# Kernel optimization log

Hardware: AMD Instinct MI355X
Metric: run time of the kernel (lower is better)

## Reference

```python
import jax, jax.numpy as jnp
import numpy as np

N = 100000      # nodes (size_src == size_dst)
E = 1_600_000   # edges, avg degree 16
IN = 128
HID = 128
OUT = 64
DROP_P = 0.5


def setup_inputs() -> dict:
    key = jax.random.key(0)
    ks = jax.random.split(key, 10)
    x = jax.random.normal(ks[0], (N, IN), dtype=jnp.float32)
    edge = jax.random.randint(ks[1], (2, E), 0, N, dtype=jnp.int32)
    # CuGraphSAGEConv: Linear(2*in_channels -> out_channels) over concat([agg, x]), with bias
    def lin_init(k, fan_in, fan_out):
        return jax.random.normal(k, (fan_in, fan_out), dtype=jnp.float32) / np.sqrt(fan_in)
    w0 = lin_init(ks[2], 2 * IN, HID); b0 = jnp.zeros((HID,), jnp.float32)
    w1 = lin_init(ks[3], 2 * HID, HID); b1 = jnp.zeros((HID,), jnp.float32)
    w2 = lin_init(ks[4], 2 * HID, HID); b2 = jnp.zeros((HID,), jnp.float32)
    lin_w = lin_init(ks[5], HID, OUT); lin_b = jnp.zeros((OUT,), jnp.float32)
    return {"x": x, "edge": edge, "w0": w0, "b0": b0, "w1": w1, "b1": b1,
            "w2": w2, "b2": b2, "lin_w": lin_w, "lin_b": lin_b,
            "size_src": N, "size_dst": N}


def _mean_agg(h, src, dst, n):
    # mean over incoming neighbors: agg[i] = mean_{(s->i) in E} h[s]
    msg = jnp.take(h, src, axis=0)                      # [E, d]
    s = jax.ops.segment_sum(msg, dst, num_segments=n)   # [n, d]
    deg = jax.ops.segment_sum(jnp.ones((src.shape[0],), h.dtype), dst, num_segments=n)
    return s / jnp.maximum(deg, 1.0)[:, None]


def _sage_layer(h, src, dst, n_dst, w, b, drop_key):
    agg = _mean_agg(h, src, dst, h.shape[0])            # [n, d]
    z = jnp.concatenate([agg, h], axis=-1) @ w + b      # [n, out]
    z = z[:n_dst]
    z = jax.nn.relu(z)
    keep = jax.random.bernoulli(drop_key, 1.0 - DROP_P, z.shape)
    return jnp.where(keep, z / (1.0 - DROP_P), 0.0)


def reference(x, edge, w0, b0, w1, b1, w2, b2, lin_w, lin_b, size_src, size_dst):
    src, dst = edge[0], edge[1]
    dkey = jax.random.key(42)
    h = x
    for i, (w, b) in enumerate([(w0, b0), (w1, b1), (w2, b2)]):
        h = _sage_layer(h, src, dst, size_dst, w, b, jax.random.fold_in(dkey, i))
    return h @ lin_w + lin_b
```

## Files before the change

### kernel.cpp

```cpp
#include <hip/hip_runtime.h>
#include <stdint.h>

#define NN 100000
#define NE 1600000
#define NFLAT 12800000u
#define XRANGE 12500
#define XCHUNKS 782
#define GBLK 782
#define MAXDEG 64

typedef _Float16 f16;
typedef __attribute__((ext_vector_type(2))) _Float16 f16x2;
typedef __attribute__((ext_vector_type(4))) _Float16 f16x4;
typedef __attribute__((ext_vector_type(8))) _Float16 f16x8;
typedef __attribute__((ext_vector_type(4))) float f32x4;

__device__ __forceinline__ uint32_t rotl32(uint32_t x, int r) {
  return __builtin_amdgcn_alignbit(x, x, (32 - r) & 31);
}

__device__ __forceinline__ void tf2x32(uint32_t k0, uint32_t k1,
                                       uint32_t x0, uint32_t x1,
                                       uint32_t &o0, uint32_t &o1) {
  uint32_t ks2 = k0 ^ k1 ^ 0x1BD11BDAu;
#define TF_R(r) { x0 += x1; x1 = rotl32(x1, r); x1 ^= x0; }
  x0 += k0; x1 += k1;
  TF_R(13) TF_R(15) TF_R(26) TF_R(6)
  x0 += k1;  x1 += ks2 + 1u;
  TF_R(17) TF_R(29) TF_R(16) TF_R(24)
  x0 += ks2; x1 += k0 + 2u;
  TF_R(13) TF_R(15) TF_R(26) TF_R(6)
  x0 += k0;  x1 += k1 + 3u;
  TF_R(17) TF_R(29) TF_R(16) TF_R(24)
  x0 += k1;  x1 += ks2 + 4u;
  TF_R(13) TF_R(15) TF_R(26) TF_R(6)
  x0 += ks2; x1 += k0 + 5u;
#undef TF_R
  o0 = x0; o1 = x1;
}

static void tf2x32_host(uint32_t k0, uint32_t k1, uint32_t x0, uint32_t x1,
                        uint32_t *o0, uint32_t *o1) {
  uint32_t ks2 = k0 ^ k1 ^ 0x1BD11BDAu;
#define TF_R(r) { x0 += x1; x1 = (x1 << (r)) | (x1 >> (32 - (r))); x1 ^= x0; }
  x0 += k0; x1 += k1;
  TF_R(13) TF_R(15) TF_R(26) TF_R(6)
  x0 += k1;  x1 += ks2 + 1u;
  TF_R(17) TF_R(29) TF_R(16) TF_R(24)
  x0 += ks2; x1 += k0 + 2u;
  TF_R(13) TF_R(15) TF_R(26) TF_R(6)
  x0 += k0;  x1 += k1 + 3u;
  TF_R(17) TF_R(29) TF_R(16) TF_R(24)
  x0 += k1;  x1 += ks2 + 4u;
  TF_R(13) TF_R(15) TF_R(26) TF_R(6)
  x0 += ks2; x1 += k0 + 5u;
#undef TF_R
  *o0 = x0; *o1 = x1;
}

__global__ __launch_bounds__(256) void fill_xcd(const int *__restrict__ src,
                                                const int *__restrict__ dst,
                                                int *__restrict__ cursor,
                                                int *__restrict__ col2) {
  int x = blockIdx.x & 7;
  int chunk = blockIdx.x >> 3;
  int lo = x * XRANGE, hi = lo + XRANGE;
  int base = chunk * 2048 + threadIdx.x;
#pragma unroll
  for (int t = 0; t < 8; ++t) {
    int e = base + t * 256;
    if (e < NE) {
      int d = dst[e];
      if (d >= lo && d < hi) {
        int p = atomicAdd(&cursor[d], 1);
        if (p < MAXDEG) col2[d * MAXDEG + p] = src[e];
      }
    }
  }
}

__global__ __launch_bounds__(256) void cvt_x_kernel(const float *__restrict__ x,
                                                    f16 *__restrict__ xh) {
  uint32_t i = (blockIdx.x * 256 + threadIdx.x) * 4;
  float4 v = *(const float4 *)(x + i);
  f16x4 o;
  o[0] = (f16)v.x; o[1] = (f16)v.y; o[2] = (f16)v.z; o[3] = (f16)v.w;
  *(f16x4 *)(xh + i) = o;
}

__global__ __launch_bounds__(256) void cvt_w_kernel(
    const float *__restrict__ w0, const float *__restrict__ w1,
    const float *__restrict__ w2, const float *__restrict__ lw,
    f16 *__restrict__ Wk0, f16 *__restrict__ Wk1, f16 *__restrict__ Wk2,
    f16 *__restrict__ WkL) {
  int t = blockIdx.x * 256 + threadIdx.x;
  if (t < 3 * 32768) {
    int wi = t >> 15, r = t & 32767;
    int k = r >> 7, c = r & 127;
    const float *w = (wi == 0) ? w0 : ((wi == 1) ? w1 : w2);
    f16 *o = (wi == 0) ? Wk0 : ((wi == 1) ? Wk1 : Wk2);
    o[c * 256 + k] = (f16)w[r];
  } else {
    int r = t - 3 * 32768;
    int k = r >> 6, c = r & 63;
    WkL[c * 128 + k] = (f16)lw[r];
  }
}

__global__ __launch_bounds__(256) void agg_kernel(const f16 *__restrict__ h,
                                                  const int *__restrict__ deg,
                                                  const int *__restrict__ col2,
                                                  f16 *__restrict__ agg,
                                                  uint32_t *__restrict__ mrow,
                                                  uint32_t mk0, uint32_t mk1) {
  int wid = threadIdx.x >> 6;
  int lane = threadIdx.x & 63;
  int n = (blockIdx.x & 7) * XRANGE + (blockIdx.x >> 3) * 4 + wid;

  {
    uint32_t j0 = (uint32_t)n * 128u + (uint32_t)lane;
    uint32_t o0, o1, p0, p1;
    tf2x32(mk0, mk1, 0u, j0, o0, o1);
    tf2x32(mk0, mk1, 0u, j0 + 64u, p0, p1);
    unsigned long long blo = __ballot((int)(o0 ^ o1) >= 0);
    unsigned long long bhi = __ballot((int)(p0 ^ p1) >= 0);
    if (lane == 0) {
      uint4 mv;
      mv.x = (uint32_t)blo; mv.y = (uint32_t)(blo >> 32);
      mv.z = (uint32_t)bhi; mv.w = (uint32_t)(bhi >> 32);
      *(uint4 *)(mrow + (size_t)n * 4) = mv;
    }
  }

  const int beg = n * MAXDEG;
  int d = min(deg[n], MAXDEG);
  const int q4 = lane >> 4;
  const int r = lane & 15;
  float s0 = 0.f, s1 = 0.f, s2 = 0.f, s3 = 0.f;
  float s4 = 0.f, s5 = 0.f, s6 = 0.f, s7 = 0.f;
  int i = 0;
  for (; i + 8 <= d; i += 8) {
    int c0 = col2[beg + i + q4];
    int c1 = col2[beg + i + 4 + q4];
    f16x8 v0 = ((const f16x8 *)(h + (size_t)c0 * 128))[r];
    f16x8 v1 = ((const f16x8 *)(h + (size_t)c1 * 128))[r];
    s0 += (float)v0[0] + (float)v1[0];
    s1 += (float)v0[1] + (float)v1[1];
    s2 += (float)v0[2] + (float)v1[2];
    s3 += (float)v0[3] + (float)v1[3];
    s4 += (float)v0[4] + (float)v1[4];
    s5 += (float)v0[5] + (float)v1[5];
    s6 += (float)v0[6] + (float)v1[6];
    s7 += (float)v0[7] + (float)v1[7];
  }
  for (; i + 4 <= d; i += 4) {
    int c = col2[beg + i + q4];
    f16x8 v = ((const f16x8 *)(h + (size_t)c * 128))[r];
    s0 += (float)v[0]; s1 += (float)v[1];
    s2 += (float)v[2]; s3 += (float)v[3];
    s4 += (float)v[4]; s5 += (float)v[5];
    s6 += (float)v[6]; s7 += (float)v[7];
  }
  if (i < d && q4 < d - i) {
    int c = col2[beg + i + q4];
    f16x8 v = ((const f16x8 *)(h + (size_t)c * 128))[r];
    s0 += (float)v[0]; s1 += (float)v[1];
    s2 += (float)v[2]; s3 += (float)v[3];
    s4 += (float)v[4]; s5 += (float)v[5];
    s6 += (float)v[6]; s7 += (float)v[7];
  }
  s0 += __shfl_xor(s0, 16); s0 += __shfl_xor(s0, 32);
  s1 += __shfl_xor(s1, 16); s1 += __shfl_xor(s1, 32);
  s2 += __shfl_xor(s2, 16); s2 += __shfl_xor(s2, 32);
  s3 += __shfl_xor(s3, 16); s3 += __shfl_xor(s3, 32);
  s4 += __shfl_xor(s4, 16); s4 += __shfl_xor(s4, 32);
  s5 += __shfl_xor(s5, 16); s5 += __shfl_xor(s5, 32);
  s6 += __shfl_xor(s6, 16); s6 += __shfl_xor(s6, 32);
  s7 += __shfl_xor(s7, 16); s7 += __shfl_xor(s7, 32);
  if (q4 == 0) {
    float inv = 1.0f / (float)max(d, 1);
    f16x8 o;
    o[0] = (f16)(s0 * inv); o[1] = (f16)(s1 * inv);
    o[2] = (f16)(s2 * inv); o[3] = (f16)(s3 * inv);
    o[4] = (f16)(s4 * inv); o[5] = (f16)(s5 * inv);
    o[6] = (f16)(s6 * inv); o[7] = (f16)(s7 * inv);
    ((f16x8 *)(agg + (size_t)n * 128))[r] = o;
  }
}

__global__ __launch_bounds__(256) void sage_gemm_f16(
    const f16 *__restrict__ agg, const f16 *__restrict__ hin,
    const f16 *__restrict__ Wk, const float *__restrict__ bias,
    const uint32_t *__restrict__ mask, f16 *__restrict__ hout) {
  const int tid = threadIdx.x;
  const int lane = tid & 63;
  const int wv = tid >> 6;
  const int blk_row0 = blockIdx.x * 128;
  const int kg = (lane >> 4) * 8;
  const int col_lo = lane & 15;

  f16x8 Bf[2][8];
#pragma unroll
  for (int t = 0; t < 2; ++t) {
    const int colb = wv * 32 + t * 16 + col_lo;
#pragma unroll
    for (int ks = 0; ks < 8; ++ks)
      Bf[t][ks] = *(const f16x8 *)(Wk + (size_t)colb * 256 + ks * 32 + kg);
  }
  const float bv0 = bias[wv * 32 + col_lo];
  const float bv1 = bias[wv * 32 + 16 + col_lo];

#pragma unroll 2
  for (int s = 0; s < 8; ++s) {
    const int row0 = blk_row0 + s * 16;
    const int ar = row0 + col_lo;
    const bool rowok = ar < NN;
    f16x8 Af[8];
#pragma unroll
    for (int ks = 0; ks < 8; ++ks) {
      const f16 *asrc = (ks < 4)
                            ? (agg + (size_t)ar * 128 + ks * 32 + kg)
                            : (hin + (size_t)ar * 128 + (ks - 4) * 32 + kg);
      Af[ks] = rowok ? *(const f16x8 *)asrc : (f16x8){};
    }
    f32x4 acc0 = {0.f, 0.f, 0.f, 0.f}, acc1 = {0.f, 0.f, 0.f, 0.f};
#pragma unroll
    for (int ks = 0; ks < 8; ++ks) {
      acc0 = __builtin_amdgcn_mfma_f32_16x16x32_f16(Af[ks], Bf[0][ks], acc0, 0, 0, 0);
      acc1 = __builtin_amdgcn_mfma_f32_16x16x32_f16(Af[ks], Bf[1][ks], acc1, 0, 0, 0);
    }
    const int rbase = row0 + (lane >> 4) * 4;
    const int c0 = wv * 32 + col_lo;
    const int c1 = c0 + 16;
#pragma unroll
    for (int r = 0; r < 4; ++r) {
      const int row = rbase + r;
      if (row < NN) {
        uint32_t mw = mask[(size_t)row * 4 + wv];
        float z0 = acc0[r] + bv0;
        float z1 = acc1[r] + bv1;
        z0 = (z0 > 0.f && ((mw >> col_lo) & 1u)) ? z0 * 2.f : 0.f;
        z1 = (z1 > 0.f && ((mw >> (16 + col_lo)) & 1u)) ? z1 * 2.f : 0.f;
        hout[(size_t)row * 128 + c0] = (f16)z0;
        hout[(size_t)row * 128 + c1] = (f16)z1;
      }
    }
  }
}

__global__ __launch_bounds__(256) void final_gemm_f16(
    const f16 *__restrict__ hin, const f16 *__restrict__ WkL,
    const float *__restrict__ bias, float *__restrict__ outp) {
  const int tid = threadIdx.x;
  const int lane = tid & 63;
  const int wv = tid >> 6;
  const int blk_row0 = blockIdx.x * 128;
  const int kg = (lane >> 4) * 8;
  const int col_lo = lane & 15;
  const int c = wv * 16 + col_lo;
  f16x8 Bf[4];
#pragma unroll
  for (int ks = 0; ks < 4; ++ks)
    Bf[ks] = *(const f16x8 *)(WkL + (size_t)c * 128 + ks * 32 + kg);
  const float bv = bias[c];
#pragma unroll 2
  for (int s = 0; s < 8; ++s) {
    const int row0 = blk_row0 + s * 16;
    const int ar = row0 + col_lo;
    const bool rowok = ar < NN;
    f32x4 acc = {0.f, 0.f, 0.f, 0.f};
#pragma unroll
    for (int ks = 0; ks < 4; ++ks) {
      f16x8 a = rowok
                    ? *(const f16x8 *)(hin + (size_t)ar * 128 + ks * 32 + kg)
                    : (f16x8){};
      acc = __builtin_amdgcn_mfma_f32_16x16x32_f16(a, Bf[ks], acc, 0, 0, 0);
    }
    const int rbase = row0 + (lane >> 4) * 4;
#pragma unroll
    for (int r = 0; r < 4; ++r) {
      const int row = rbase + r;
      if (row < NN) outp[(size_t)row * 64 + c] = acc[r] + bv;
    }
  }
}

extern "C" void kernel_launch(void *const *d_in, const int *in_sizes, int n_in,
                              void *d_out, int out_size, void *d_ws,
                              size_t ws_size, hipStream_t stream) {
  (void)in_sizes; (void)n_in; (void)out_size; (void)ws_size;
  const float *x = (const float *)d_in[0];
  const int *edge = (const int *)d_in[1];
  const int *src = edge;
  const int *dst = edge + NE;
  const float *w0 = (const float *)d_in[2];
  const float *b0 = (const float *)d_in[3];
  const float *w1 = (const float *)d_in[4];
  const float *b1 = (const float *)d_in[5];
  const float *w2 = (const float *)d_in[6];
  const float *b2 = (const float *)d_in[7];
  const float *lw = (const float *)d_in[8];
  const float *lb = (const float *)d_in[9];
  float *out = (float *)d_out;

  char *ws = (char *)d_ws;
  f16 *xh  = (f16 *)ws; ws += (size_t)NN * 128 * 2;
  f16 *h1  = (f16 *)ws; ws += (size_t)NN * 128 * 2;
  f16 *h2  = (f16 *)ws; ws += (size_t)NN * 128 * 2;
  f16 *agg = (f16 *)ws; ws += (size_t)NN * 128 * 2;
  f16 *Wk0 = (f16 *)ws; ws += 256 * 128 * 2;
  f16 *Wk1 = (f16 *)ws; ws += 256 * 128 * 2;
  f16 *Wk2 = (f16 *)ws; ws += 256 * 128 * 2;
  f16 *WkL = (f16 *)ws; ws += 128 * 64 * 2;
  int *cursor = (int *)ws; ws += (size_t)NN * 4;
  int *col2 = (int *)ws;   ws += (size_t)NN * MAXDEG * 4;
  uint32_t *m0 = (uint32_t *)ws; ws += (size_t)(NFLAT / 32) * 4;
  uint32_t *m1 = (uint32_t *)ws; ws += (size_t)(NFLAT / 32) * 4;
  uint32_t *m2 = (uint32_t *)ws; ws += (size_t)(NFLAT / 32) * 4;

  uint32_t fk[3][2];
  for (int i = 0; i < 3; ++i)
    tf2x32_host(0u, 42u, 0u, (uint32_t)i, &fk[i][0], &fk[i][1]);

  hipMemsetAsync(cursor, 0, (size_t)NN * 4, stream);
  fill_xcd<<<8 * XCHUNKS, 256, 0, stream>>>(src, dst, cursor, col2);
  cvt_x_kernel<<<NFLAT / 1024, 256, 0, stream>>>(x, xh);
  cvt_w_kernel<<<416, 256, 0, stream>>>(w0, w1, w2, lw, Wk0, Wk1, Wk2, WkL);

  agg_kernel<<<NN / 4, 256, 0, stream>>>(xh, cursor, col2, agg, m0,
                                         fk[0][0], fk[0][1]);
  sage_gemm_f16<<<GBLK, 256, 0, stream>>>(agg, xh, Wk0, b0, m0, h1);
  agg_kernel<<<NN / 4, 256, 0, stream>>>(h1, cursor, col2, agg, m1,
                                         fk[1][0], fk[1][1]);
  sage_gemm_f16<<<GBLK, 256, 0, stream>>>(agg, h1, Wk1, b1, m1, h2);
  agg_kernel<<<NN / 4, 256, 0, stream>>>(h2, cursor, col2, agg, m2,
                                         fk[2][0], fk[2][1]);
  sage_gemm_f16<<<GBLK, 256, 0, stream>>>(agg, h2, Wk2, b2, m2, xh);
  final_gemm_f16<<<GBLK, 256, 0, stream>>>(xh, WkL, lb, out);
}
```

Baseline: 445.3 us.

## Merge prep kernels, fuse final linear into last SAGE GEMM via LDS

Combines the CSR fill, x conversion and weight conversion kernels into one launch partitioned by block index. The final output GEMM is fused into the last SAGE layer's GEMM: the layer-3 activations are staged in shared memory and multiplied by the output weights in the same block, so they are never written to or reread from global memory. The aggregation kernel also gains a 16-neighbor unrolled loop to keep more gathers in flight. Costs are extra LDS use and a block barrier in the fused kernel, plus possible register pressure from the wider unroll.

```diff
diff --git a/kernel.cpp b/kernel.cpp
--- a/kernel.cpp
+++ b/kernel.cpp
@@ -8,6 +8,10 @@
 #define XCHUNKS 782
 #define GBLK 782
 #define MAXDEG 64
+#define FILLB (8 * XCHUNKS)
+#define CVTXB 12500
+#define CVTWB 416
+#define LDSW 136
 
 typedef _Float16 f16;
 typedef __attribute__((ext_vector_type(2))) _Float16 f16x2;
@@ -58,52 +62,51 @@
   *o0 = x0; *o1 = x1;
 }
 
-__global__ __launch_bounds__(256) void fill_xcd(const int *__restrict__ src,
-                                                const int *__restrict__ dst,
-                                                int *__restrict__ cursor,
-                                                int *__restrict__ col2) {
-  int x = blockIdx.x & 7;
-  int chunk = blockIdx.x >> 3;
-  int lo = x * XRANGE, hi = lo + XRANGE;
-  int base = chunk * 2048 + threadIdx.x;
-#pragma unroll
-  for (int t = 0; t < 8; ++t) {
-    int e = base + t * 256;
-    if (e < NE) {
-      int d = dst[e];
-      if (d >= lo && d < hi) {
-        int p = atomicAdd(&cursor[d], 1);
-        if (p < MAXDEG) col2[d * MAXDEG + p] = src[e];
-      }
-    }
-  }
-}
-
-__global__ __launch_bounds__(256) void cvt_x_kernel(const float *__restrict__ x,
-                                                    f16 *__restrict__ xh) {
-  uint32_t i = (blockIdx.x * 256 + threadIdx.x) * 4;
-  float4 v = *(const float4 *)(x + i);
-  f16x4 o;
-  o[0] = (f16)v.x; o[1] = (f16)v.y; o[2] = (f16)v.z; o[3] = (f16)v.w;
-  *(f16x4 *)(xh + i) = o;
-}
-
-__global__ __launch_bounds__(256) void cvt_w_kernel(
+__global__ __launch_bounds__(256) void prep_kernel(
+    const int *__restrict__ src, const int *__restrict__ dst,
+    int *__restrict__ cursor, int *__restrict__ col2,
+    const float *__restrict__ x, f16 *__restrict__ xh,
     const float *__restrict__ w0, const float *__restrict__ w1,
     const float *__restrict__ w2, const float *__restrict__ lw,
     f16 *__restrict__ Wk0, f16 *__restrict__ Wk1, f16 *__restrict__ Wk2,
     f16 *__restrict__ WkL) {
-  int t = blockIdx.x * 256 + threadIdx.x;
-  if (t < 3 * 32768) {
-    int wi = t >> 15, r = t & 32767;
-    int k = r >> 7, c = r & 127;
-    const float *w = (wi == 0) ? w0 : ((wi == 1) ? w1 : w2);
-    f16 *o = (wi == 0) ? Wk0 : ((wi == 1) ? Wk1 : Wk2);
-    o[c * 256 + k] = (f16)w[r];
+  const int bid = blockIdx.x;
+  const int tid = threadIdx.x;
+  if (bid < FILLB) {
+    int xr = bid & 7;
+    int chunk = bid >> 3;
+    int lo = xr * XRANGE, hi = lo + XRANGE;
+    int base = chunk * 2048 + tid;
+#pragma unroll
+    for (int t = 0; t < 8; ++t) {
+      int e = base + t * 256;
+      if (e < NE) {
+        int d = dst[e];
+        if (d >= lo && d < hi) {
+          int p = atomicAdd(&cursor[d], 1);
+          if (p < MAXDEG) col2[d * MAXDEG + p] = src[e];
+        }
+      }
+    }
+  } else if (bid < FILLB + CVTXB) {
+    uint32_t i = (uint32_t)(bid - FILLB) * 1024u + (uint32_t)tid * 4u;
+    float4 v = *(const float4 *)(x + i);
+    f16x4 o;
+    o[0] = (f16)v.x; o[1] = (f16)v.y; o[2] = (f16)v.z; o[3] = (f16)v.w;
+    *(f16x4 *)(xh + i) = o;
   } else {
-    int r = t - 3 * 32768;
-    int k = r >> 6, c = r & 63;
-    WkL[c * 128 + k] = (f16)lw[r];
+    int t = (bid - FILLB - CVTXB) * 256 + tid;
+    if (t < 3 * 32768) {
+      int wi = t >> 15, r = t & 32767;
+      int k = r >> 7, c = r & 127;
+      const float *w = (wi == 0) ? w0 : ((wi == 1) ? w1 : w2);
+      f16 *o = (wi == 0) ? Wk0 : ((wi == 1) ? Wk1 : Wk2);
+      o[c * 256 + k] = (f16)w[r];
+    } else {
+      int r = t - 3 * 32768;
+      int k = r >> 6, c = r & 63;
+      WkL[c * 128 + k] = (f16)lw[r];
+    }
   }
 }
 
@@ -139,6 +142,24 @@
   float s0 = 0.f, s1 = 0.f, s2 = 0.f, s3 = 0.f;
   float s4 = 0.f, s5 = 0.f, s6 = 0.f, s7 = 0.f;
   int i = 0;
+  for (; i + 16 <= d; i += 16) {
+    int c0 = col2[beg + i + q4];
+    int c1 = col2[beg + i + 4 + q4];
+    int c2 = col2[beg + i + 8 + q4];
+    int c3 = col2[beg + i + 12 + q4];
+    f16x8 v0 = ((const f16x8 *)(h + (size_t)c0 * 128))[r];
+    f16x8 v1 = ((const f16x8 *)(h + (size_t)c1 * 128))[r];
+    f16x8 v2 = ((const f16x8 *)(h + (size_t)c2 * 128))[r];
+    f16x8 v3 = ((const f16x8 *)(h + (size_t)c3 * 128))[r];
+    s0 += (float)v0[0] + (float)v1[0] + (float)v2[0] + (float)v3[0];
+    s1 += (float)v0[1] + (float)v1[1] + (float)v2[1] + (float)v3[1];
+    s2 += (float)v0[2] + (float)v1[2] + (float)v2[2] + (float)v3[2];
+    s3 += (float)v0[3] + (float)v1[3] + (float)v2[3] + (float)v3[3];
+    s4 += (float)v0[4] + (float)v1[4] + (float)v2[4] + (float)v3[4];
+    s5 += (float)v0[5] + (float)v1[5] + (float)v2[5] + (float)v3[5];
+    s6 += (float)v0[6] + (float)v1[6] + (float)v2[6] + (float)v3[6];
+    s7 += (float)v0[7] + (float)v1[7] + (float)v2[7] + (float)v3[7];
+  }
   for (; i + 8 <= d; i += 8) {
     int c0 = col2[beg + i + q4];
     int c1 = col2[beg + i + 4 + q4];
@@ -188,10 +209,15 @@
   }
 }
 
+template <int FINAL>
 __global__ __launch_bounds__(256) void sage_gemm_f16(
     const f16 *__restrict__ agg, const f16 *__restrict__ hin,
     const f16 *__restrict__ Wk, const float *__restrict__ bias,
-    const uint32_t *__restrict__ mask, f16 *__restrict__ hout) {
+    const uint32_t *__restrict__ mask, f16 *__restrict__ hout,
+    const f16 *__restrict__ WkL, const float *__restrict__ lb,
+    float *__restrict__ outp) {
+  extern __shared__ char smem[];
+  f16 (*hl)[LDSW] = (f16(*)[LDSW])smem;
   const int tid = threadIdx.x;
   const int lane = tid & 63;
   const int wv = tid >> 6;
@@ -231,7 +257,6 @@
     }
     const int rbase = row0 + (lane >> 4) * 4;
     const int c0 = wv * 32 + col_lo;
-    const int c1 = c0 + 16;
 #pragma unroll
     for (int r = 0; r < 4; ++r) {
       const int row = rbase + r;
@@ -241,46 +266,41 @@
         float z1 = acc1[r] + bv1;
         z0 = (z0 > 0.f && ((mw >> col_lo) & 1u)) ? z0 * 2.f : 0.f;
         z1 = (z1 > 0.f && ((mw >> (16 + col_lo)) & 1u)) ? z1 * 2.f : 0.f;
-        hout[(size_t)row * 128 + c0] = (f16)z0;
-        hout[(size_t)row * 128 + c1] = (f16)z1;
+        if constexpr (FINAL) {
+          const int lr = row - blk_row0;
+          hl[lr][c0] = (f16)z0;
+          hl[lr][c0 + 16] = (f16)z1;
+        } else {
+          hout[(size_t)row * 128 + c0] = (f16)z0;
+          hout[(size_t)row * 128 + c0 + 16] = (f16)z1;
+        }
       }
     }
   }
-}
-
-__global__ __launch_bounds__(256) void final_gemm_f16(
-    const f16 *__restrict__ hin, const f16 *__restrict__ WkL,
-    const float *__restrict__ bias, float *__restrict__ outp) {
-  const int tid = threadIdx.x;
-  const int lane = tid & 63;
-  const int wv = tid >> 6;
-  const int blk_row0 = blockIdx.x * 128;
-  const int kg = (lane >> 4) * 8;
-  const int col_lo = lane & 15;
-  const int c = wv * 16 + col_lo;
-  f16x8 Bf[4];
-#pragma unroll
-  for (int ks = 0; ks < 4; ++ks)
-    Bf[ks] = *(const f16x8 *)(WkL + (size_t)c * 128 + ks * 32 + kg);
-  const float bv = bias[c];
+
+  if constexpr (FINAL) {
+    __syncthreads();
+    const int c = wv * 16 + col_lo;
+    f16x8 Bf2[4];
+#pragma unroll
+    for (int ks = 0; ks < 4; ++ks)
+      Bf2[ks] = *(const f16x8 *)(WkL + (size_t)c * 128 + ks * 32 + kg);
+    const float bv = lb[c];
 #pragma unroll 2
-  for (int s = 0; s < 8; ++s) {
-    const int row0 = blk_row0 + s * 16;
-    const int ar = row0 + col_lo;
-    const bool rowok = ar < NN;
-    f32x4 acc = {0.f, 0.f, 0.f, 0.f};
-#pragma unroll
-    for (int ks = 0; ks < 4; ++ks) {
-      f16x8 a = rowok
-                    ? *(const f16x8 *)(hin + (size_t)ar * 128 + ks * 32 + kg)
-                    : (f16x8){};
-      acc = __builtin_amdgcn_mfma_f32_16x16x32_f16(a, Bf[ks], acc, 0, 0, 0);
-    }
-    const int rbase = row0 + (lane >> 4) * 4;
-#pragma unroll
-    for (int r = 0; r < 4; ++r) {
-      const int row = rbase + r;
-      if (row < NN) outp[(size_t)row * 64 + c] = acc[r] + bv;
+    for (int s = 0; s < 8; ++s) {
+      const int lr = s * 16 + col_lo;
+      f32x4 acc = {0.f, 0.f, 0.f, 0.f};
+#pragma unroll
+      for (int ks = 0; ks < 4; ++ks) {
+        f16x8 a = *(const f16x8 *)&hl[lr][ks * 32 + kg];
+        acc = __builtin_amdgcn_mfma_f32_16x16x32_f16(a, Bf2[ks], acc, 0, 0, 0);
+      }
+      const int rbase = blk_row0 + s * 16 + (lane >> 4) * 4;
+#pragma unroll
+      for (int r = 0; r < 4; ++r) {
+        const int row = rbase + r;
+        if (row < NN) outp[(size_t)row * 64 + c] = acc[r] + bv;
+      }
     }
   }
 }
@@ -323,18 +343,19 @@
     tf2x32_host(0u, 42u, 0u, (uint32_t)i, &fk[i][0], &fk[i][1]);
 
   hipMemsetAsync(cursor, 0, (size_t)NN * 4, stream);
-  fill_xcd<<<8 * XCHUNKS, 256, 0, stream>>>(src, dst, cursor, col2);
-  cvt_x_kernel<<<NFLAT / 1024, 256, 0, stream>>>(x, xh);
-  cvt_w_kernel<<<416, 256, 0, stream>>>(w0, w1, w2, lw, Wk0, Wk1, Wk2, WkL);
+  prep_kernel<<<FILLB + CVTXB + CVTWB, 256, 0, stream>>>(
+      src, dst, cursor, col2, x, xh, w0, w1, w2, lw, Wk0, Wk1, Wk2, WkL);
 
   agg_kernel<<<NN / 4, 256, 0, stream>>>(xh, cursor, col2, agg, m0,
                                          fk[0][0], fk[0][1]);
-  sage_gemm_f16<<<GBLK, 256, 0, stream>>>(agg, xh, Wk0, b0, m0, h1);
+  sage_gemm_f16<0><<<GBLK, 256, 0, stream>>>(agg, xh, Wk0, b0, m0, h1,
+                                             nullptr, nullptr, nullptr);
   agg_kernel<<<NN / 4, 256, 0, stream>>>(h1, cursor, col2, agg, m1,
                                          fk[1][0], fk[1][1]);
-  sage_gemm_f16<<<GBLK, 256, 0, stream>>>(agg, h1, Wk1, b1, m1, h2);
+  sage_gemm_f16<0><<<GBLK, 256, 0, stream>>>(agg, h1, Wk1, b1, m1, h2,
+                                             nullptr, nullptr, nullptr);
   agg_kernel<<<NN / 4, 256, 0, stream>>>(h2, cursor, col2, agg, m2,
                                          fk[2][0], fk[2][1]);
-  sage_gemm_f16<<<GBLK, 256, 0, stream>>>(agg, h2, Wk2, b2, m2, xh);
-  final_gemm_f16<<<GBLK, 256, 0, stream>>>(xh, WkL, lb, out);
-}
+  sage_gemm_f16<1><<<GBLK, 256, 128 * LDSW * 2, stream>>>(
+      agg, h2, Wk2, b2, m2, nullptr, WkL, lb, out);
+}
```

Measured after the change: 415.8 us. 6.6% less time.
